# Optimization experiments

Hardware: AMD Instinct MI355X
Metric: run time of the kernel (lower is better)

The kernel has to match this reference:

```python
import jax, jax.numpy as jnp
import numpy as np

B, L, D = 8, 4096, 128
TEMPERATURE = 1.0


def setup_inputs() -> dict:
    key = jax.random.key(0)
    kx, kw, kb = jax.random.split(key, 3)
    x = jax.random.normal(kx, (B, L, D), dtype=jnp.float32)
    # nn.Linear(dim, dim): weight [D, D], bias [D]
    bound = 1.0 / np.sqrt(D)
    W = jax.random.uniform(kw, (D, D), minval=-bound, maxval=bound, dtype=jnp.float32)
    b = jax.random.uniform(kb, (D,), minval=-bound, maxval=bound, dtype=jnp.float32)
    return {"x": x, "W": W, "b": b}


def reference(x, W, b):
    # projected = proj(x): torch Linear is x @ W.T + b
    projected = jnp.einsum("bld,ed->ble", x, W) + b            # [B, L, D]

    # adaptive_avg_pool1d over sequence length L -> L//2 (L even => pair means)
    Bq, Lx, Dx = x.shape
    q = x.reshape(Bq, Lx // 2, 2, Dx).mean(axis=2)             # [B, L/2, D]
    q = jnp.einsum("bld,ed->ble", q, W) + b                    # [B, L/2, D]

    # pairwise squared euclidean distance via ||q||^2 + ||k||^2 - 2 q.k (GEMM form)
    q_sq = jnp.sum(q * q, axis=-1, keepdims=True)              # [B, L/2, 1]
    k_sq = jnp.sum(projected * projected, axis=-1)[:, None, :] # [B, 1, L]
    qk = jnp.einsum("bqd,bkd->bqk", q, projected)              # [B, L/2, L]
    power = jnp.maximum(q_sq + k_sq - 2.0 * qk, 0.0)
    distances = jnp.sqrt(power)
    similarities = jnp.exp(-distances * TEMPERATURE)           # [B, L/2, L]

    k = jnp.einsum("bqk,bkd->bqd", similarities, projected)    # [B, L/2, D]
    v = k
    return (q, k, v)
```

## Files before the change

### kernel.cpp

```cpp
#include <hip/hip_runtime.h>
#include <hip/hip_bf16.h>
#include <stdint.h>

#define NB 8
#define LL 4096
#define LQ 2048
#define DD 128

typedef __attribute__((ext_vector_type(8))) short short8;
typedef __attribute__((ext_vector_type(4))) short short4v;
typedef __attribute__((ext_vector_type(4))) float f4;
typedef __attribute__((ext_vector_type(2))) unsigned int u2;

typedef const __attribute__((address_space(1))) unsigned int guint_t;
typedef __attribute__((address_space(3))) unsigned int luint_t;

__device__ __forceinline__ short8 pack8(const float* v) {
    __hip_bfloat16 h[8];
    #pragma unroll
    for (int j = 0; j < 8; ++j) h[j] = __float2bfloat16(v[j]);
    return *(short8*)h;
}

__global__ __launch_bounds__(256) void projA_kernel(
    const float* __restrict__ x, const float* __restrict__ W,
    const float* __restrict__ bias,
    __hip_bfloat16* __restrict__ proj_sw, __hip_bfloat16* __restrict__ projT_sw,
    __hip_bfloat16* __restrict__ qb, float* __restrict__ qf,
    float* __restrict__ psq, float* __restrict__ qsq)
{
    __shared__ __hip_bfloat16 Wlds[128 * 128];
    __shared__ __hip_bfloat16 Tt[4][128 * 16];

    const int tid = threadIdx.x;
    const int lane = tid & 63, w = tid >> 6;
    const int lr = lane & 15, lh = lane >> 4;

    #pragma unroll
    for (int k = 0; k < 16; ++k) {
        const int f = k * 1024 + tid * 4;
        const int e = f >> 7, col = f & 127;
        f4 v = *(const f4*)&W[f];
        __hip_bfloat16 h[4];
        #pragma unroll
        for (int j = 0; j < 4; ++j) h[j] = __float2bfloat16(v[j]);
        const int byte = e * 256 + (((col * 2)) ^ ((e & 7) << 4));
        *(u2*)((char*)Wlds + byte) = *(u2*)h;
    }
    float bv[8];
    #pragma unroll
    for (int nt = 0; nt < 8; ++nt) bv[nt] = bias[nt * 16 + lr];
    __syncthreads();

    const int tile = blockIdx.x;
    const int row0 = tile * 64 + w * 16;
    const bool qmode = tile >= (NB * LL / 64);

    short8 a[4];
    if (!qmode) {
        const float* src = x + (size_t)(row0 + lr) * DD;
        #pragma unroll
        for (int ks = 0; ks < 4; ++ks) {
            float t[8];
            *(f4*)&t[0] = *(const f4*)&src[ks * 32 + lh * 8];
            *(f4*)&t[4] = *(const f4*)&src[ks * 32 + lh * 8 + 4];
            a[ks] = pack8(t);
        }
    } else {
        const int gq = row0 - NB * LL + lr;
        const int b = gq >> 11, l = gq & 2047;
        const float* s0 = x + ((size_t)b * LL + 2 * l) * DD;
        #pragma unroll
        for (int ks = 0; ks < 4; ++ks) {
            float t[8];
            f4 u0 = *(const f4*)&s0[ks * 32 + lh * 8];
            f4 u1 = *(const f4*)&s0[ks * 32 + lh * 8 + 4];
            f4 v0 = *(const f4*)&s0[DD + ks * 32 + lh * 8];
            f4 v1 = *(const f4*)&s0[DD + ks * 32 + lh * 8 + 4];
            *(f4*)&t[0] = (u0 + v0) * 0.5f;
            *(f4*)&t[4] = (u1 + v1) * 0.5f;
            a[ks] = pack8(t);
        }
    }

    f4 acc[8] = {};
    #pragma unroll
    for (int nt = 0; nt < 8; ++nt) {
        const int e = nt * 16 + lr;
        #pragma unroll
        for (int ks = 0; ks < 4; ++ks) {
            const int byte = e * 256 + ((ks * 64 + lh * 16) ^ ((lr & 7) << 4));
            short8 bk = *(const short8*)((char*)Wlds + byte);
            acc[nt] = __builtin_amdgcn_mfma_f32_16x16x32_bf16(a[ks], bk, acc[nt], 0, 0, 0);
        }
    }

    __hip_bfloat16 h[8][4];
    f4 rn = {0.f, 0.f, 0.f, 0.f};
    #pragma unroll
    for (int nt = 0; nt < 8; ++nt)
        #pragma unroll
        for (int r = 0; r < 4; ++r) {
            float v = acc[nt][r] + bv[nt];
            acc[nt][r] = v;
            h[nt][r] = __float2bfloat16(v);
            float vb = __bfloat162float(h[nt][r]);
            rn[r] += vb * vb;
        }
    #pragma unroll
    for (int m = 1; m < 16; m <<= 1) {
        #pragma unroll
        for (int r = 0; r < 4; ++r) rn[r] += __shfl_xor(rn[r], m);
    }

    if (!qmode) {
        const int gr = row0;
        #pragma unroll
        for (int nt = 0; nt < 8; ++nt)
            #pragma unroll
            for (int r = 0; r < 4; ++r) {
                const int row = gr + lh * 4 + r;
                const int byte = (nt * 32 + lr * 2) ^ (((lh * 4 + r) & 7) << 4);
                *(__hip_bfloat16*)((char*)proj_sw + (size_t)row * 256 + byte) =
                    __float2bfloat16(-2.0f * __bfloat162float(h[nt][r]));
            }
        if (lr == 0) *(f4*)&psq[gr + lh * 4] = rn;
        #pragma unroll
        for (int nt = 0; nt < 8; ++nt) {
            __hip_bfloat16 p[4] = {h[nt][0], h[nt][1], h[nt][2], h[nt][3]};
            *(u2*)((char*)&Tt[w][0] + (nt * 16 + lr) * 32 + lh * 8) = *(u2*)p;
        }
        const int b = gr >> 12, l0 = gr & 4095;
        #pragma unroll
        for (int i = 0; i < 2; ++i) {
            const int e = lane + i * 64;
            const int sw = (e & 15) << 3;
            char* rowbase = (char*)projT_sw + ((size_t)(b * DD + e)) * (LL * 2)
                          + (size_t)(l0 & ~63) * 2;
            const int ob = (l0 & 63) * 2;
            #pragma unroll
            for (int c = 0; c < 4; ++c) {
                u2 chunk = *(u2*)((char*)&Tt[w][e * 16] + c * 8);
                *(u2*)(rowbase + ((ob + c * 8) ^ sw)) = chunk;
            }
        }
    } else {
        const int gq = row0 - NB * LL;
        #pragma unroll
        for (int nt = 0; nt < 8; ++nt)
            #pragma unroll
            for (int r = 0; r < 4; ++r) {
                const size_t idx = (size_t)(gq + lh * 4 + r) * DD + nt * 16 + lr;
                qb[idx] = h[nt][r];
                qf[idx] = acc[nt][r];
            }
        if (lr == 0) *(f4*)&qsq[gq + lh * 4] = rn;
    }
}

__global__ __launch_bounds__(512, 2) void fused_kernel(
    const __hip_bfloat16* __restrict__ proj_sw, const __hip_bfloat16* __restrict__ projT_sw,
    const __hip_bfloat16* __restrict__ qb, const float* __restrict__ psq,
    const float* __restrict__ qsq,
    float* __restrict__ pp0, float* __restrict__ pp1,
    float* __restrict__ pp2, float* __restrict__ pp3, int keys_per)
{
    __shared__ __hip_bfloat16 pbuf[2][8192];
    __shared__ __hip_bfloat16 tbuf[2][8192];
    __shared__ __align__(16) float psbuf[2048];

    const int bid = blockIdx.x;
    const int b = bid & 7;
    const int qt8 = (bid >> 3) & 7;
    const int ks = bid >> 6;
    const int tid = threadIdx.x;
    const int w = tid >> 6, lane = tid & 63;
    const int lr = lane & 15, lh = lane >> 4;

    const int qrow0 = qt8 * 256 + w * 32;
    const int key0 = ks * keys_per;
    const int ntiles = keys_per / 64;

    const char* psw = (const char*)proj_sw + (size_t)b * LL * 256;
    const char* ptbsw = (const char*)projT_sw + (size_t)b * DD * LL * 2;
    const float* psb = psq + b * LL;

    for (int i = tid; i < keys_per; i += 512) psbuf[i] = psb[key0 + i];

    short8 aq[2][4];
    const __hip_bfloat16* qbase = qb + ((size_t)b * LQ + qrow0) * DD;
    #pragma unroll
    for (int mt = 0; mt < 2; ++mt)
        #pragma unroll
        for (int kss = 0; kss < 4; ++kss)
            aq[mt][kss] = *(const short8*)&qbase[(size_t)(mt * 16 + lr) * DD + kss * 32 + lh * 8];
    const float qn0 = qsq[b * LQ + qrow0 + lr];
    const float qn1 = qsq[b * LQ + qrow0 + 16 + lr];

    __syncthreads();

    const char* sp = psw + (size_t)key0 * 256 + w * 2048;
    const char* st = ptbsw + (size_t)(w * 16 + (lane >> 3)) * (LL * 2)
                   + (size_t)key0 * 2 + (lane & 7) * 16;
    auto stage = [&](int buf) {
        #pragma unroll
        for (int j = 0; j < 2; ++j)
            __builtin_amdgcn_global_load_lds(
                (guint_t*)(sp + j * 1024 + lane * 16),
                (luint_t*)&pbuf[buf][w * 1024 + j * 512 + lane * 8], 16, 0, 0);
        #pragma unroll
        for (int j = 0; j < 2; ++j)
            __builtin_amdgcn_global_load_lds(
                (guint_t*)(st + (size_t)j * 8 * (LL * 2)),
                (luint_t*)&tbuf[buf][(w * 16 + j * 8) * 64 + lane * 8], 16, 0, 0);
        sp += 64 * 256;
        st += 64 * 2;
    };

    stage(0);
    stage(1);

    f4 oc[2][8] = {};
    int p = 0;

    for (int t = 0; t < ntiles; ++t) {
        if (t + 1 < ntiles) asm volatile("s_waitcnt vmcnt(4)" ::: "memory");
        else                asm volatile("s_waitcnt vmcnt(0)" ::: "memory");
        asm volatile("s_barrier" ::: "memory");

        #pragma unroll
        for (int sub = 0; sub < 2; ++sub) {
            f4 pn0 = *(const f4*)&psbuf[t * 64 + sub * 32 + lh * 4];
            f4 pn1 = *(const f4*)&psbuf[t * 64 + sub * 32 + 16 + lh * 4];
            f4 s00, s01, s10, s11;
            #pragma unroll
            for (int r = 0; r < 4; ++r) {
                s00[r] = qn0 + pn0[r];  s01[r] = qn1 + pn0[r];
                s10[r] = qn0 + pn1[r];  s11[r] = qn1 + pn1[r];
            }
            __builtin_amdgcn_s_setprio(1);
            #pragma unroll
            for (int kss = 0; kss < 4; ++kss) {
                const int off = (kss * 64 + lh * 16) ^ ((lr & 7) << 4);
                short8 ak0 = *(const short8*)((const char*)pbuf[p] + (sub * 32 + lr) * 256 + off);
                short8 ak1 = *(const short8*)((const char*)pbuf[p] + (sub * 32 + 16 + lr) * 256 + off);
                s00 = __builtin_amdgcn_mfma_f32_16x16x32_bf16(ak0, aq[0][kss], s00, 0, 0, 0);
                s01 = __builtin_amdgcn_mfma_f32_16x16x32_bf16(ak0, aq[1][kss], s01, 0, 0, 0);
                s10 = __builtin_amdgcn_mfma_f32_16x16x32_bf16(ak1, aq[0][kss], s10, 0, 0, 0);
                s11 = __builtin_amdgcn_mfma_f32_16x16x32_bf16(ak1, aq[1][kss], s11, 0, 0, 0);
            }
            __builtin_amdgcn_s_setprio(0);

            short8 pa0, pa1;
            {
                alignas(16) __hip_bfloat16 hh[8];
                #pragma unroll
                for (int r = 0; r < 4; ++r) {
                    hh[r]     = __float2bfloat16(__expf(-__builtin_amdgcn_sqrtf(fmaxf(s00[r], 0.0f))));
                    hh[4 + r] = __float2bfloat16(__expf(-__builtin_amdgcn_sqrtf(fmaxf(s10[r], 0.0f))));
                }
                pa0 = *(short8*)hh;
                #pragma unroll
                for (int r = 0; r < 4; ++r) {
                    hh[r]     = __float2bfloat16(__expf(-__builtin_amdgcn_sqrtf(fmaxf(s01[r], 0.0f))));
                    hh[4 + r] = __float2bfloat16(__expf(-__builtin_amdgcn_sqrtf(fmaxf(s11[r], 0.0f))));
                }
                pa1 = *(short8*)hh;
            }

            __builtin_amdgcn_s_setprio(1);
            #pragma unroll
            for (int dt = 0; dt < 8; ++dt) {
                const char* rowp = (const char*)tbuf[p] + (dt * 16 + lr) * 128;
                const int sw = lr << 3;
                union { short8 v; short4v h[2]; } u;
                u.h[0] = *(const short4v*)(rowp + ((lh * 8 + sub * 64) ^ sw));
                u.h[1] = *(const short4v*)(rowp + ((lh * 8 + 32 + sub * 64) ^ sw));
                oc[0][dt] = __builtin_amdgcn_mfma_f32_16x16x32_bf16(pa0, u.v, oc[0][dt], 0, 0, 0);
                oc[1][dt] = __builtin_amdgcn_mfma_f32_16x16x32_bf16(pa1, u.v, oc[1][dt], 0, 0, 0);
            }
            __builtin_amdgcn_s_setprio(0);
        }

        asm volatile("s_barrier" ::: "memory");
        if (t + 2 < ntiles) stage(p);
        p ^= 1;
    }

    float* pb = (ks == 0) ? pp0 : (ks == 1) ? pp1 : (ks == 2) ? pp2 : pp3;
    #pragma unroll
    for (int mt = 0; mt < 2; ++mt)
        #pragma unroll
        for (int dt = 0; dt < 8; ++dt)
            #pragma unroll
            for (int r = 0; r < 4; ++r)
                pb[((size_t)b * LQ + qrow0 + mt * 16 + lh * 4 + r) * DD + dt * 16 + lr]
                    = oc[mt][dt][r];
}

__global__ __launch_bounds__(256) void reduce_kernel(
    const float* __restrict__ p0, const float* __restrict__ p1,
    const float* __restrict__ p2, const float* __restrict__ p3,
    float* __restrict__ outk, float* __restrict__ outv, int nsplit)
{
    const int b = blockIdx.x & 7;
    const size_t j = (size_t)b * (LQ * DD) + ((size_t)(blockIdx.x >> 3) * 256 + threadIdx.x) * 4;
    f4 v = *(const f4*)&p0[j] + *(const f4*)&p1[j];
    if (nsplit == 4) v += *(const f4*)&p2[j] + *(const f4*)&p3[j];
    *(f4*)&outk[j] = v;
    *(f4*)&outv[j] = v;
}

extern "C" void kernel_launch(void* const* d_in, const int* in_sizes, int n_in,
                              void* d_out, int out_size, void* d_ws, size_t ws_size,
                              hipStream_t stream) {
    const float* x = (const float*)d_in[0];
    const float* W = (const float*)d_in[1];
    const float* bias = (const float*)d_in[2];

    float* out = (float*)d_out;
    const size_t NQ = (size_t)NB * LQ * DD;
    float* qf = out;
    float* outk = out + NQ;
    float* outv = out + 2 * NQ;

    char* ws = (char*)d_ws;
    __hip_bfloat16* proj  = (__hip_bfloat16*)ws;
    __hip_bfloat16* projT = (__hip_bfloat16*)(ws + 8u * 1024 * 1024);
    __hip_bfloat16* qb    = (__hip_bfloat16*)(ws + 16u * 1024 * 1024);
    float* psq            = (float*)(ws + 20u * 1024 * 1024);
    float* qsq            = (float*)(ws + 20u * 1024 * 1024 + 256u * 1024);
    float* pw2            = (float*)(ws + 24u * 1024 * 1024);
    float* pw3            = (float*)(ws + 32u * 1024 * 1024);

    const int nsplit = (ws_size >= (40ull << 20)) ? 4 : 2;
    const int keys_per = LL / nsplit;

    hipLaunchKernelGGL(projA_kernel, dim3((NB * LL + NB * LQ) / 64), dim3(256), 0, stream,
                       x, W, bias, proj, projT, qb, qf, psq, qsq);
    hipLaunchKernelGGL(fused_kernel, dim3(64 * nsplit), dim3(512), 0, stream,
                       proj, projT, qb, psq, qsq, outk, outv, pw2, pw3, keys_per);
    hipLaunchKernelGGL(reduce_kernel, dim3(2048), dim3(256), 0, stream,
                       outk, outv, pw2, pw3, outk, outv, nsplit);
}
```

Measured before the change: 77.03 us.

## Fuse split-K reduction into fused kernel via last-block atomic counter

```diff
diff --git a/kernel.cpp b/kernel.cpp
--- a/kernel.cpp
+++ b/kernel.cpp
@@ -27,7 +27,7 @@
     const float* __restrict__ bias,
     __hip_bfloat16* __restrict__ proj_sw, __hip_bfloat16* __restrict__ projT_sw,
     __hip_bfloat16* __restrict__ qb, float* __restrict__ qf,
-    float* __restrict__ psq, float* __restrict__ qsq)
+    float* __restrict__ psq, float* __restrict__ qsq, int* __restrict__ ctr)
 {
     __shared__ __hip_bfloat16 Wlds[128 * 128];
     __shared__ __hip_bfloat16 Tt[4][128 * 16];
@@ -35,6 +35,8 @@
     const int tid = threadIdx.x;
     const int lane = tid & 63, w = tid >> 6;
     const int lr = lane & 15, lh = lane >> 4;
+
+    if (blockIdx.x == 0 && tid < 64) ctr[tid] = 0;
 
     #pragma unroll
     for (int k = 0; k < 16; ++k) {
@@ -163,11 +165,14 @@
     const __hip_bfloat16* __restrict__ qb, const float* __restrict__ psq,
     const float* __restrict__ qsq,
     float* __restrict__ pp0, float* __restrict__ pp1,
-    float* __restrict__ pp2, float* __restrict__ pp3, int keys_per)
+    float* __restrict__ pp2, float* __restrict__ pp3,
+    float* __restrict__ outk, float* __restrict__ outv,
+    int* __restrict__ ctr, int keys_per, int nsplit)
 {
     __shared__ __hip_bfloat16 pbuf[2][8192];
     __shared__ __hip_bfloat16 tbuf[2][8192];
     __shared__ __align__(16) float psbuf[2048];
+    __shared__ int lastflag;
 
     const int bid = blockIdx.x;
     const int b = bid & 7;
@@ -296,19 +301,26 @@
             for (int r = 0; r < 4; ++r)
                 pb[((size_t)b * LQ + qrow0 + mt * 16 + lh * 4 + r) * DD + dt * 16 + lr]
                     = oc[mt][dt][r];
-}
-
-__global__ __launch_bounds__(256) void reduce_kernel(
-    const float* __restrict__ p0, const float* __restrict__ p1,
-    const float* __restrict__ p2, const float* __restrict__ p3,
-    float* __restrict__ outk, float* __restrict__ outv, int nsplit)
-{
-    const int b = blockIdx.x & 7;
-    const size_t j = (size_t)b * (LQ * DD) + ((size_t)(blockIdx.x >> 3) * 256 + threadIdx.x) * 4;
-    f4 v = *(const f4*)&p0[j] + *(const f4*)&p1[j];
-    if (nsplit == 4) v += *(const f4*)&p2[j] + *(const f4*)&p3[j];
-    *(f4*)&outk[j] = v;
-    *(f4*)&outv[j] = v;
+
+    __threadfence();
+    __syncthreads();
+    if (tid == 0) {
+        int old = __hip_atomic_fetch_add(&ctr[b * 8 + qt8], 1,
+                                         __ATOMIC_ACQ_REL, __HIP_MEMORY_SCOPE_AGENT);
+        lastflag = (old == nsplit - 1) ? 1 : 0;
+    }
+    __syncthreads();
+    if (lastflag) {
+        __threadfence();
+        const size_t base = (size_t)b * (LQ * DD) + (size_t)qt8 * 256 * DD;
+        for (int i = tid; i < 8192; i += 512) {
+            const size_t j = base + (size_t)i * 4;
+            f4 v = *(const f4*)&pp0[j] + *(const f4*)&pp1[j];
+            if (nsplit == 4) v += *(const f4*)&pp2[j] + *(const f4*)&pp3[j];
+            *(f4*)&outk[j] = v;
+            *(f4*)&outv[j] = v;
+        }
+    }
 }
 
 extern "C" void kernel_launch(void* const* d_in, const int* in_sizes, int n_in,
@@ -330,16 +342,16 @@
     __hip_bfloat16* qb    = (__hip_bfloat16*)(ws + 16u * 1024 * 1024);
     float* psq            = (float*)(ws + 20u * 1024 * 1024);
     float* qsq            = (float*)(ws + 20u * 1024 * 1024 + 256u * 1024);
-    float* pw2            = (float*)(ws + 24u * 1024 * 1024);
-    float* pw3            = (float*)(ws + 32u * 1024 * 1024);
+    int*   ctr            = (int*)(ws + 21u * 1024 * 1024);
+    float* pw0            = (float*)(ws + 24u * 1024 * 1024);
+    float* pw1            = (float*)(ws + 32u * 1024 * 1024);
 
     const int nsplit = (ws_size >= (40ull << 20)) ? 4 : 2;
     const int keys_per = LL / nsplit;
 
     hipLaunchKernelGGL(projA_kernel, dim3((NB * LL + NB * LQ) / 64), dim3(256), 0, stream,
-                       x, W, bias, proj, projT, qb, qf, psq, qsq);
+                       x, W, bias, proj, projT, qb, qf, psq, qsq, ctr);
     hipLaunchKernelGGL(fused_kernel, dim3(64 * nsplit), dim3(512), 0, stream,
-                       proj, projT, qb, psq, qsq, outk, outv, pw2, pw3, keys_per);
-    hipLaunchKernelGGL(reduce_kernel, dim3(2048), dim3(256), 0, stream,
-                       outk, outv, pw2, pw3, outk, outv, nsplit);
+                       proj, projT, qb, psq, qsq,
+                       outk, outv, pw0, pw1, outk, outv, ctr, keys_per, nsplit);
 }
```

Measured after the change: 154.7 us. 101% more time.
